# Optimization experiments

Hardware: AMD Instinct MI355X
Metric: run time of the kernel (lower is better)

Reference implementation:

```python
import jax, jax.numpy as jnp
import numpy as np

DIM = 1024
NHEADS = 16
DIM_HEAD = 64
HIDDEN = NHEADS * DIM_HEAD  # 1024


def _xavier(key, fan_in, fan_out):
    limit = np.sqrt(6.0 / (fan_in + fan_out))
    return jax.random.uniform(key, (fan_in, fan_out), jnp.float32, -limit, limit)


def setup_inputs() -> dict:
    key = jax.random.key(0)
    kq, k1, k2, k3 = jax.random.split(key, 4)
    q = jax.random.normal(kq, (2, 2048, DIM), jnp.float32)
    Wq = _xavier(k1, DIM, HIDDEN)
    bq = jnp.zeros((HIDDEN,), jnp.float32)
    Wkv = _xavier(k2, DIM, 2 * HIDDEN)
    bkv = jnp.zeros((2 * HIDDEN,), jnp.float32)
    Wo = _xavier(k3, HIDDEN, DIM)
    bo = jnp.zeros((DIM,), jnp.float32)
    return {"q": q, "Wq": Wq, "bq": bq, "Wkv": Wkv, "bkv": bkv, "Wo": Wo, "bo": bo}


def reference(q, Wq, bq, Wkv, bkv, Wo, bo):
    scale = DIM_HEAD ** (-0.5)
    query = q @ Wq + bq                      # [b, s, hidden]
    kv = q @ Wkv + bkv                       # self-attention: kv from q
    key_, value = jnp.split(kv, 2, axis=-1)  # [b, s, hidden] each
    b, s, _ = query.shape
    query = query.reshape(b, s, NHEADS, DIM_HEAD)
    key_ = key_.reshape(b, s, NHEADS, DIM_HEAD)
    value = value.reshape(b, s, NHEADS, DIM_HEAD)
    scores = jnp.einsum('bqhd,bkhd->bhqk', query, key_) * scale
    attn = jax.nn.softmax(scores, axis=-1)
    out = jnp.einsum('bhqk,bkhd->bqhd', attn, value)
    out = out.reshape(b, s, HIDDEN)
    return out @ Wo + bo
```

## Files before the change

### kernel.cpp

```cpp
#include <hip/hip_runtime.h>

#define DIM 1024
#define NHEADS 16
#define DH 64
#define BATCH 2
#define SEQ 2048

typedef float f32x4 __attribute__((ext_vector_type(4)));
typedef short s16x8 __attribute__((ext_vector_type(8)));
typedef short s16x4 __attribute__((ext_vector_type(4)));

__device__ __forceinline__ short f2bf(float f) {
    union { float f; unsigned u; } v; v.f = f;
    unsigned r = v.u + 0x7fffu + ((v.u >> 16) & 1u);
    return (short)(r >> 16);
}

#if defined(__has_builtin)
#if __has_builtin(__builtin_amdgcn_cvt_pk_bf16_f32)
#define HAVE_PK_BF16 1
#endif
#endif
__device__ __forceinline__ unsigned f2bf_pk(float a, float b) {
#ifdef HAVE_PK_BF16
    typedef __bf16 bf16x2_t __attribute__((ext_vector_type(2)));
    bf16x2_t r = __builtin_amdgcn_cvt_pk_bf16_f32(a, b);
    return __builtin_bit_cast(unsigned, r);
#else
    return ((unsigned)(unsigned short)f2bf(b) << 16) | (unsigned short)f2bf(a);
#endif
}
__device__ __forceinline__ s16x4 pk4(float a, float b, float c, float d) {
    union { unsigned u[2]; s16x4 v; } x;
    x.u[0] = f2bf_pk(a, b); x.u[1] = f2bf_pk(c, d);
    return x.v;
}

#if defined(__has_builtin)
#if __has_builtin(__builtin_amdgcn_exp2f)
#define EXP2(x) __builtin_amdgcn_exp2f(x)
#endif
#endif
#ifndef EXP2
#define EXP2(x) exp2f(x)
#endif

__device__ __forceinline__ void gld16(const void* g, void* l) {
    __builtin_amdgcn_global_load_lds(
        (const __attribute__((address_space(1))) void*)g,
        (__attribute__((address_space(3))) void*)l, 16, 0, 0);
}

__global__ __launch_bounds__(256) void prep_kernel(
    const float* __restrict__ X, short* __restrict__ Y,
    const float* __restrict__ Wq, const float* __restrict__ Wkv,
    const float* __restrict__ Wo, short* __restrict__ WT)
{
    const int t = threadIdx.x;
    if (blockIdx.x < 2048) {
        const int i = (blockIdx.x * 256 + t) * 8;
        float4 a = *(const float4*)(X + i);
        float4 b = *(const float4*)(X + i + 4);
        union { unsigned u[4]; s16x8 v; } o;
        o.u[0] = f2bf_pk(a.x, a.y); o.u[1] = f2bf_pk(a.z, a.w);
        o.u[2] = f2bf_pk(b.x, b.y); o.u[3] = f2bf_pk(b.z, b.w);
        *(s16x8*)(Y + i) = o.v;
    } else {
        const int i2 = blockIdx.x - 2048;
        const int bx = i2 & 63, by = i2 >> 6;
        const int ng = bx * 64 + (t & 63);
        const int k0 = (by * 4 + (t >> 6)) * 8;
        const float* W; int n, N;
        if (ng < 1024)      { W = Wq;  n = ng;        N = 1024; }
        else if (ng < 3072) { W = Wkv; n = ng - 1024; N = 2048; }
        else                { W = Wo;  n = ng - 3072; N = 1024; }
        float v[8];
#pragma unroll
        for (int j = 0; j < 8; ++j) v[j] = W[(size_t)(k0 + j) * N + n];
        union { unsigned u[4]; s16x8 s; } o;
        o.u[0] = f2bf_pk(v[0], v[1]); o.u[1] = f2bf_pk(v[2], v[3]);
        o.u[2] = f2bf_pk(v[4], v[5]); o.u[3] = f2bf_pk(v[6], v[7]);
        *(s16x8*)&WT[(size_t)ng * 1024 + k0] = o.s;
    }
}

__global__ __launch_bounds__(256) void transpose_v_kernel(
    const short* __restrict__ QKV, short* __restrict__ VtG)
{
    const int t = threadIdx.x;
    const int tok0 = blockIdx.x * 64;
    const int h = blockIdx.y, b = blockIdx.z;
    __shared__ short L[64 * 72];
    const short* src = QKV + (size_t)(b * SEQ + tok0) * 3072 + 2048 + h * 64;
#pragma unroll
    for (int p = 0; p < 2; ++p) {
        int r = p * 32 + (t >> 3);
        *(s16x8*)&L[r * 72 + (t & 7) * 8] = *(const s16x8*)(src + (size_t)r * 3072 + (t & 7) * 8);
    }
    __syncthreads();
    short* dst = VtG + (size_t)(b * NHEADS + h) * 64 * SEQ + tok0;
#pragma unroll
    for (int p = 0; p < 2; ++p) {
        int u = p * 256 + t;
        int dv = u >> 3, c = (u & 7) * 8;
        s16x8 o;
#pragma unroll
        for (int j = 0; j < 8; ++j) o[j] = L[(c + j) * 72 + dv];
        *(s16x8*)(dst + (size_t)dv * SEQ + c) = o;
    }
}

template<int TM, bool OUT_BF16>
__global__ __launch_bounds__(256) void gemm_mfma_kernel(
    const short* __restrict__ A, const short* __restrict__ Bt,
    const float* __restrict__ bias0, const float* __restrict__ bias1, int nsplit,
    float s0, float s1, void* __restrict__ C, int M, int N)
{
    const int K = 1024;
    constexpr int NI = (TM == 128) ? 4 : 2;
    __shared__ short As[TM * 32];
    __shared__ short Bs[128 * 32];

    const int t    = threadIdx.x;
    const int wave = t >> 6;
    const int lane = t & 63;
    const int col  = lane & 15;
    const int quad = lane >> 4;
    const int m0 = blockIdx.y * TM;
    const int n0 = blockIdx.x * 128;
    const int wroff = (TM == 128) ? (wave >> 1) * 64 : 0;
    const int wcoff = (TM == 128) ? (wave & 1) * 64 : wave * 32;

    f32x4 acc[4][NI];
#pragma unroll
    for (int mi = 0; mi < 4; ++mi)
#pragma unroll
        for (int ni = 0; ni < NI; ++ni) acc[mi][ni] = (f32x4){0.f, 0.f, 0.f, 0.f};

    constexpr int RPW = TM / 4;
    const int ldrowA = wave * RPW + (lane >> 2);
    const int ldrowB = wave * 32  + (lane >> 2);
    const int ldcol  = (lane & 3) * 8;
    const short* Ag = A  + (size_t)(m0 + ldrowA) * K + ldcol;
    const short* Bg = Bt + (size_t)(n0 + ldrowB) * K + ldcol;
    short* AsW = &As[wave * RPW * 32];
    short* BsW = &Bs[wave * 1024];

    for (int k0 = 0; k0 < K; k0 += 32) {
        __syncthreads();
        gld16(Ag + k0, AsW);
        if (TM == 128) gld16(Ag + 16 * K + k0, AsW + 512);
        gld16(Bg + k0,          BsW);
        gld16(Bg + 16 * K + k0, BsW + 512);
        __syncthreads();

        s16x8 aA[4], bB[NI];
#pragma unroll
        for (int mi = 0; mi < 4; ++mi)
            aA[mi] = *(const s16x8*)&As[(wroff + 16 * mi + col) * 32 + quad * 8];
#pragma unroll
        for (int ni = 0; ni < NI; ++ni)
            bB[ni] = *(const s16x8*)&Bs[(wcoff + 16 * ni + col) * 32 + quad * 8];
#pragma unroll
        for (int mi = 0; mi < 4; ++mi)
#pragma unroll
            for (int ni = 0; ni < NI; ++ni)
                acc[mi][ni] = __builtin_amdgcn_mfma_f32_16x16x32_bf16(aA[mi], bB[ni], acc[mi][ni], 0, 0, 0);
    }

    float bias_v[NI], scale_v[NI];
#pragma unroll
    for (int ni = 0; ni < NI; ++ni) {
        int nb = n0 + wcoff + 16 * ni + col;
        bias_v[ni]  = (nb < nsplit) ? bias0[nb] : bias1[nb - nsplit];
        scale_v[ni] = (nb < nsplit) ? s0 : s1;
    }

#pragma unroll
    for (int mi = 0; mi < 4; ++mi)
#pragma unroll
        for (int ni = 0; ni < NI; ++ni)
#pragma unroll
            for (int r = 0; r < 4; ++r) {
                const int gm = m0 + wroff + 16 * mi + quad * 4 + r;
                const int gn = n0 + wcoff + 16 * ni + col;
                float v = (acc[mi][ni][r] + bias_v[ni]) * scale_v[ni];
                if (OUT_BF16) ((short*)C)[(size_t)gm * N + gn] = f2bf(v);
                else          ((float*)C)[(size_t)gm * N + gn] = v;
            }
}

__global__ __launch_bounds__(512, 4) void attn_v15_kernel(
    const short* __restrict__ QKV,
    const short* __restrict__ VtG,
    short* __restrict__ O)
{
    const int L = blockIdx.x + 16 * blockIdx.y + 256 * blockIdx.z;
    const int xcd = L & 7, idx = L >> 3;
    const int pair = xcd * 4 + (idx >> 4);
    const int qt = idx & 15;
    const int h  = pair & 15;
    const int b  = pair >> 4;
    const int t  = threadIdx.x;
    const int wave = t >> 6;
    const int lane = t & 63;
    const int col  = lane & 15;
    const int quad = lane >> 4;
    const int wq = wave & 3;
    const int kh = wave >> 2;

    __shared__ __align__(16) short Lds[28672];
    short* KsB = Lds;
    short* VtB = Lds + 2 * 64 * 72;
    short* PsW = Lds + 4 * 64 * 72 + wave * (32 * 40);

    const short* Qg = QKV + (size_t)(b * SEQ + qt * 128) * 3072 + h * DH;
    const short* Kg = QKV + (size_t)(b * SEQ) * 3072 + 1024 + h * DH;
    const short* VtRow = VtG + (size_t)(b * NHEADS + h) * 64 * SEQ;

    s16x8 aQ[2][2];
#pragma unroll
    for (int tq = 0; tq < 2; ++tq)
#pragma unroll
        for (int kq = 0; kq < 2; ++kq)
            aQ[tq][kq] = *(const s16x8*)(Qg + (size_t)(wq * 32 + 16 * tq + col) * 3072 + kq * 32 + quad * 8);

    f32x4 oa[4][2];
    float lsum[2] = {0.f, 0.f};
#pragma unroll
    for (int td = 0; td < 4; ++td)
#pragma unroll
        for (int tq = 0; tq < 2; ++tq) oa[td][tq] = (f32x4){0.f, 0.f, 0.f, 0.f};

    const int srow = t >> 3;
    const int sc8  = (t & 7) * 8;
    const short* KgS  = Kg + (size_t)srow * 3072 + sc8;
    const short* VtgS = VtRow + (size_t)srow * SEQ + sc8;
    s16x8 kx = *(const s16x8*)KgS;
    s16x8 vx = *(const s16x8*)VtgS;

    for (int kt = 0; kt < SEQ / 64; ++kt) {
        const int cur = kt & 1;
        *(s16x8*)&KsB[cur * 4608 + srow * 72 + sc8] = kx;
        *(s16x8*)&VtB[cur * 4608 + srow * 72 + sc8] = vx;
        {
            int nt = (kt + 1 < SEQ / 64) ? kt + 1 : kt;
            kx = *(const s16x8*)(KgS + (size_t)nt * 64 * 3072);
            vx = *(const s16x8*)(VtgS + (size_t)nt * 64);
        }
        __syncthreads();

        s16x8 aK[2][2];
#pragma unroll
        for (int tk = 0; tk < 2; ++tk)
#pragma unroll
            for (int kq = 0; kq < 2; ++kq)
                aK[tk][kq] = *(const s16x8*)&KsB[cur * 4608 + (kh * 32 + 16 * tk + col) * 72 + kq * 32 + quad * 8];
        f32x4 st[2][2];
        __builtin_amdgcn_s_setprio(1);
#pragma unroll
        for (int tk = 0; tk < 2; ++tk)
#pragma unroll
            for (int tq = 0; tq < 2; ++tq) {
                f32x4 a = (f32x4){0.f, 0.f, 0.f, 0.f};
                a = __builtin_amdgcn_mfma_f32_16x16x32_bf16(aK[tk][0], aQ[tq][0], a, 0, 0, 0);
                a = __builtin_amdgcn_mfma_f32_16x16x32_bf16(aK[tk][1], aQ[tq][1], a, 0, 0, 0);
                st[tk][tq] = a;
            }
        __builtin_amdgcn_s_setprio(0);

#pragma unroll
        for (int tk = 0; tk < 2; ++tk)
#pragma unroll
            for (int tq = 0; tq < 2; ++tq) {
                float p0 = EXP2(st[tk][tq][0]);
                float p1 = EXP2(st[tk][tq][1]);
                float p2 = EXP2(st[tk][tq][2]);
                float p3 = EXP2(st[tk][tq][3]);
                lsum[tq] += (p0 + p1) + (p2 + p3);
                *(s16x4*)&PsW[(16 * tq + col) * 40 + 16 * tk + quad * 4] = pk4(p0, p1, p2, p3);
            }
        asm volatile("s_waitcnt lgkmcnt(0)" ::: "memory");

        s16x8 bP[2];
#pragma unroll
        for (int tq = 0; tq < 2; ++tq)
            bP[tq] = *(const s16x8*)&PsW[(16 * tq + col) * 40 + quad * 8];
        __builtin_amdgcn_s_setprio(1);
#pragma unroll
        for (int td = 0; td < 4; ++td) {
            const int dv = 16 * td + col;
            s16x8 aV = *(const s16x8*)&VtB[cur * 4608 + dv * 72 + kh * 32 + quad * 8];
#pragma unroll
            for (int tq = 0; tq < 2; ++tq)
                oa[td][tq] = __builtin_amdgcn_mfma_f32_16x16x32_bf16(aV, bP[tq], oa[td][tq], 0, 0, 0);
        }
        __builtin_amdgcn_s_setprio(0);
    }

#pragma unroll
    for (int tq = 0; tq < 2; ++tq) {
        lsum[tq] += __shfl_xor(lsum[tq], 16);
        lsum[tq] += __shfl_xor(lsum[tq], 32);
    }

    __syncthreads();
    float* red  = (float*)Lds;
    float* redl = red + 4 * 64 * 36;
    if (wave >= 4) {
        const int slot = wave & 3;
#pragma unroll
        for (int td = 0; td < 4; ++td)
#pragma unroll
            for (int tq = 0; tq < 2; ++tq)
#pragma unroll
                for (int r = 0; r < 4; ++r)
                    red[slot * 2304 + (16 * td + quad * 4 + r) * 36 + 16 * tq + col] = oa[td][tq][r];
        if (quad == 0)
#pragma unroll
            for (int tq = 0; tq < 2; ++tq)
                redl[slot * 32 + 16 * tq + col] = lsum[tq];
    }
    __syncthreads();

    if (wave < 4) {
        const int slot = wq;
#pragma unroll
        for (int td = 0; td < 4; ++td)
#pragma unroll
            for (int tq = 0; tq < 2; ++tq)
#pragma unroll
                for (int r = 0; r < 4; ++r)
                    oa[td][tq][r] += red[slot * 2304 + (16 * td + quad * 4 + r) * 36 + 16 * tq + col];
        float inv[2];
#pragma unroll
        for (int tq = 0; tq < 2; ++tq) {
            lsum[tq] += redl[slot * 32 + 16 * tq + col];
            inv[tq] = 1.f / lsum[tq];
        }
        short* Og = O + (size_t)(b * SEQ + qt * 128 + wq * 32) * DIM + h * DH;
#pragma unroll
        for (int td = 0; td < 4; ++td)
#pragma unroll
            for (int tq = 0; tq < 2; ++tq)
                *(s16x4*)(Og + (size_t)(16 * tq + col) * DIM + 16 * td + quad * 4) =
                    pk4(oa[td][tq][0] * inv[tq], oa[td][tq][1] * inv[tq],
                        oa[td][tq][2] * inv[tq], oa[td][tq][3] * inv[tq]);
    }
}

extern "C" void kernel_launch(void* const* d_in, const int* in_sizes, int n_in,
                              void* d_out, int out_size, void* d_ws, size_t ws_size,
                              hipStream_t stream)
{
    const float* q   = (const float*)d_in[0];
    const float* Wq  = (const float*)d_in[1];
    const float* bq  = (const float*)d_in[2];
    const float* Wkv = (const float*)d_in[3];
    const float* bkv = (const float*)d_in[4];
    const float* Wo  = (const float*)d_in[5];
    const float* bo  = (const float*)d_in[6];
    float* out = (float*)d_out;

    const int M = BATCH * SEQ;

    short* qb     = (short*)d_ws;
    short* WT     = qb     + (size_t)M * DIM;
    short* QKVbuf = WT     + (size_t)4096 * DIM;
    short* AObuf  = QKVbuf + (size_t)M * 3 * DIM;
    short* VtG    = (short*)d_out;

    const float QSCALE = 0.18033688011112042f;

    prep_kernel<<<4096, 256, 0, stream>>>(q, qb, Wq, Wkv, Wo, WT);

    gemm_mfma_kernel<128, true><<<dim3(3 * DIM / 128, M / 128), 256, 0, stream>>>(
        qb, WT, bq, bkv, DIM, QSCALE, 1.0f, QKVbuf, M, 3 * DIM);
    transpose_v_kernel<<<dim3(SEQ / 64, NHEADS, BATCH), 256, 0, stream>>>(QKVbuf, VtG);
    attn_v15_kernel<<<dim3(SEQ / 128, NHEADS, BATCH), 512, 0, stream>>>(QKVbuf, VtG, AObuf);
    gemm_mfma_kernel<64, false><<<dim3(DIM / 128, M / 64), 256, 0, stream>>>(
        AObuf, WT + (size_t)3072 * 1024, bo, bo, 1 << 30, 1.0f, 1.0f, out, M, DIM);
}
```

Before: 193.3 us.

## Double GEMM K-tile to 64 and XOR-swizzle LDS layout

The projection GEMM kernel now stages a 64-wide K slice per iteration instead of 32. This halves the number of barrier pairs and loop iterations over K. The global-to-LDS loads are remapped so each row's 16-byte chunks are XOR-swizzled by row index, and the MFMA operand reads apply the same swizzle to avoid LDS bank conflicts. LDS usage doubles, which may reduce occupancy.

```diff
diff --git a/kernel.cpp b/kernel.cpp
--- a/kernel.cpp
+++ b/kernel.cpp
@@ -117,9 +117,11 @@
     float s0, float s1, void* __restrict__ C, int M, int N)
 {
     const int K = 1024;
-    constexpr int NI = (TM == 128) ? 4 : 2;
-    __shared__ short As[TM * 32];
-    __shared__ short Bs[128 * 32];
+    constexpr int NI  = (TM == 128) ? 4 : 2;
+    constexpr int BK  = 64;
+    constexpr int RPW = TM / 4;
+    __shared__ short As[TM * BK];
+    __shared__ short Bs[128 * BK];
 
     const int t    = threadIdx.x;
     const int wave = t >> 6;
@@ -137,35 +139,42 @@
 #pragma unroll
         for (int ni = 0; ni < NI; ++ni) acc[mi][ni] = (f32x4){0.f, 0.f, 0.f, 0.f};
 
-    constexpr int RPW = TM / 4;
-    const int ldrowA = wave * RPW + (lane >> 2);
-    const int ldrowB = wave * 32  + (lane >> 2);
-    const int ldcol  = (lane & 3) * 8;
-    const short* Ag = A  + (size_t)(m0 + ldrowA) * K + ldcol;
-    const short* Bg = Bt + (size_t)(n0 + ldrowB) * K + ldcol;
-    short* AsW = &As[wave * RPW * 32];
-    short* BsW = &Bs[wave * 1024];
-
-    for (int k0 = 0; k0 < K; k0 += 32) {
+    const int sgrow = lane >> 3;
+    const int sgc   = (lane & 7) ^ sgrow;
+    const short* Ag = A  + (size_t)(m0 + wave * RPW + sgrow) * K + sgc * 8;
+    const short* Bg = Bt + (size_t)(n0 + wave * 32  + sgrow) * K + sgc * 8;
+    short* AsW = &As[wave * RPW * BK];
+    short* BsW = &Bs[wave * 32 * BK];
+
+    for (int k0 = 0; k0 < K; k0 += BK) {
         __syncthreads();
-        gld16(Ag + k0, AsW);
-        if (TM == 128) gld16(Ag + 16 * K + k0, AsW + 512);
-        gld16(Bg + k0,          BsW);
-        gld16(Bg + 16 * K + k0, BsW + 512);
+#pragma unroll
+        for (int c = 0; c < RPW / 8; ++c)
+            gld16(Ag + k0 + (size_t)c * 8 * K, AsW + c * 512);
+#pragma unroll
+        for (int c = 0; c < 4; ++c)
+            gld16(Bg + k0 + (size_t)c * 8 * K, BsW + c * 512);
         __syncthreads();
 
-        s16x8 aA[4], bB[NI];
-#pragma unroll
-        for (int mi = 0; mi < 4; ++mi)
-            aA[mi] = *(const s16x8*)&As[(wroff + 16 * mi + col) * 32 + quad * 8];
-#pragma unroll
-        for (int ni = 0; ni < NI; ++ni)
-            bB[ni] = *(const s16x8*)&Bs[(wcoff + 16 * ni + col) * 32 + quad * 8];
-#pragma unroll
-        for (int mi = 0; mi < 4; ++mi)
-#pragma unroll
-            for (int ni = 0; ni < NI; ++ni)
-                acc[mi][ni] = __builtin_amdgcn_mfma_f32_16x16x32_bf16(aA[mi], bB[ni], acc[mi][ni], 0, 0, 0);
+#pragma unroll
+        for (int ks = 0; ks < 2; ++ks) {
+            s16x8 aA[4], bB[NI];
+#pragma unroll
+            for (int mi = 0; mi < 4; ++mi) {
+                const int r = wroff + 16 * mi + col;
+                aA[mi] = *(const s16x8*)&As[r * BK + (((ks * 4 + quad) ^ (r & 7)) * 8)];
+            }
+#pragma unroll
+            for (int ni = 0; ni < NI; ++ni) {
+                const int r = wcoff + 16 * ni + col;
+                bB[ni] = *(const s16x8*)&Bs[r * BK + (((ks * 4 + quad) ^ (r & 7)) * 8)];
+            }
+#pragma unroll
+            for (int mi = 0; mi < 4; ++mi)
+#pragma unroll
+                for (int ni = 0; ni < NI; ++ni)
+                    acc[mi][ni] = __builtin_amdgcn_mfma_f32_16x16x32_bf16(aA[mi], bB[ni], acc[mi][ni], 0, 0, 0);
+        }
     }
 
     float bias_v[NI], scale_v[NI];
```

New measurement: 195.8 us. About the same (+1.3%).
